# Performance work log

Measured on AMD Instinct MI355X. Metric: run time of the kernel, lower is better.

The kernel has to match this reference:

```python
import jax, jax.numpy as jnp
import numpy as np

N, FIN, HID, HEADS, DHEAD = 4096, 512, 256, 4, 256
TOPK = 29  # hard-coded t=29 in HAN1.forward
FOUT = HEADS * DHEAD  # 1024


def setup_inputs() -> dict:
    key = jax.random.key(0)
    ks = jax.random.split(key, 12)
    h = jax.random.normal(ks[0], (N, FIN), dtype=jnp.float32)
    simlar = jax.random.normal(ks[1], (N, N), dtype=jnp.float32)
    # binary adjacency, avg degree ~41 so top-k (29) actually prunes
    adj = (jax.random.uniform(ks[2], (N, N)) < 0.01).astype(jnp.float32)
    s = 0.05
    W_trans = jax.random.normal(ks[3], (FIN, HID), dtype=jnp.float32) * s
    gat_W = jax.random.normal(ks[4], (HID, FOUT), dtype=jnp.float32) * s
    attn_l = jax.random.normal(ks[5], (HEADS, DHEAD), dtype=jnp.float32) * s
    attn_r = jax.random.normal(ks[6], (HEADS, DHEAD), dtype=jnp.float32) * s
    gat_bias = jnp.zeros((FOUT,), dtype=jnp.float32)
    sem_W1 = jax.random.normal(ks[7], (FOUT, 128), dtype=jnp.float32) * s
    sem_b1 = jnp.zeros((128,), dtype=jnp.float32)
    sem_W2 = jax.random.normal(ks[8], (128, 1), dtype=jnp.float32) * s
    return {"h": h, "simlar": simlar, "adj": adj, "W_trans": W_trans,
            "gat_W": gat_W, "attn_l": attn_l, "attn_r": attn_r,
            "gat_bias": gat_bias, "sem_W1": sem_W1, "sem_b1": sem_b1,
            "sem_W2": sem_W2}


def reference(h, simlar, adj, W_trans, gat_W, attn_l, attn_r, gat_bias,
              sem_W1, sem_b1, sem_W2):
    lrelu01 = lambda x: jax.nn.leaky_relu(x, 0.01)  # nn.LeakyReLU default
    # ---- adjacency sparsification: per-row top-k of filtered similarity ----
    filt = lrelu01(adj * simlar) * (adj > 0).astype(adj.dtype)  # [N,N]
    top_vals, top_idx = jax.lax.top_k(filt, TOPK)               # [N,TOPK]
    rows = jnp.arange(N)[:, None]
    newmat = jnp.zeros_like(filt).at[rows, top_idx].set(top_vals)
    mask = newmat != 0  # mask[src, dst]: edge src->dst (nonzero() semantics)
    # ---- feature transform (dropout p=0 -> identity) ----
    x = lrelu01(h @ W_trans)                                    # [N,HID]
    # ---- GATConv (DGL semantics, negative_slope=0.2, activation=elu) ----
    feat = (x @ gat_W).reshape(N, HEADS, DHEAD)                 # [N,H,D]
    el = jnp.einsum('nhd,hd->nh', feat, attn_l)                 # src scores
    er = jnp.einsum('nhd,hd->nh', feat, attn_r)                 # dst scores
    e = jax.nn.leaky_relu(el[:, None, :] + er[None, :, :], 0.2) # [src,dst,H]
    mask3 = mask[:, :, None]
    e = jnp.where(mask3, e, jnp.asarray(-1e30, e.dtype))
    emax = jnp.max(e, axis=0, keepdims=True)
    exp_e = jnp.where(mask3, jnp.exp(e - emax), 0.0)
    denom = jnp.sum(exp_e, axis=0, keepdims=True)
    alpha = exp_e / jnp.maximum(denom, 1e-20)  # zero-in-degree -> zero output
    rst = jnp.einsum('sdh,shf->dhf', alpha, feat)               # [N,H,D]
    rst = jax.nn.elu(rst + gat_bias.reshape(HEADS, DHEAD))
    sem = rst.reshape(N, FOUT)                                  # flatten(1)
    # ---- semantic attention over meta-paths (here: 1 meta-path) ----
    z = sem[:, None, :]                                         # [N,1,F]
    w = (jnp.tanh(z @ sem_W1 + sem_b1) @ sem_W2).mean(0)        # [1,1]
    beta = jax.nn.softmax(w, axis=0)                            # [1,1]
    out = (beta[None, :, :] * z).sum(1)                         # [N,F]
    return out
```

## Files before the change

### kernel.cpp

```cpp
#include <hip/hip_runtime.h>
#include <hip/hip_bf16.h>
#include <math.h>

#define N 4096
#define FIN 512
#define HID 256
#define HEADS 4
#define DHEAD 256
#define FOUT 1024
#define TOPK 29
#define CAP 64
#define CAPC 96

typedef __attribute__((ext_vector_type(8))) short short8;
typedef __attribute__((ext_vector_type(4))) float f32x4;
typedef __hip_bfloat16 bf16;

__device__ __forceinline__ float bflo(unsigned int u) {
  return __uint_as_float(u << 16);
}
__device__ __forceinline__ float bfhi(unsigned int u) {
  return __uint_as_float(u & 0xffff0000u);
}

__global__ __launch_bounds__(256) void prep_kernel(
    const float* __restrict__ h, const float* __restrict__ W_trans,
    const float* __restrict__ gat_W, const float* __restrict__ attn_l,
    const float* __restrict__ attn_r, bf16* __restrict__ hb,
    bf16* __restrict__ Wtb, bf16* __restrict__ gWtb,
    float* __restrict__ alr2, int* __restrict__ colcnt) {
  const int S1 = 4096;
  const int S2 = S1 + N * FIN / 4;
  const int S3 = S2 + HID * FIN / 4;
  const int S4 = S3 + FOUT * HID / 4;
  const int TOT = S4 + 2 * HEADS * HID * 16;
  const int stride = gridDim.x * 256;
  for (int i = blockIdx.x * 256 + threadIdx.x; i < TOT; i += stride) {
    if (i < S1) {
      colcnt[i] = 0;
    } else if (i < S2) {
      const int j = i - S1;
      const float4 v = reinterpret_cast<const float4*>(h)[j];
      bf16 tmp[4];
      tmp[0] = __float2bfloat16(v.x);
      tmp[1] = __float2bfloat16(v.y);
      tmp[2] = __float2bfloat16(v.z);
      tmp[3] = __float2bfloat16(v.w);
      *reinterpret_cast<ushort4*>(&hb[(size_t)j * 4]) =
          *reinterpret_cast<ushort4*>(tmp);
    } else if (i < S3) {
      const int j4 = i - S2;
      const float4 v = reinterpret_cast<const float4*>(W_trans)[j4];
      const int k = j4 >> 6;
      const int c0 = (j4 & 63) * 4;
      Wtb[(size_t)(c0 + 0) * FIN + k] = __float2bfloat16(v.x);
      Wtb[(size_t)(c0 + 1) * FIN + k] = __float2bfloat16(v.y);
      Wtb[(size_t)(c0 + 2) * FIN + k] = __float2bfloat16(v.z);
      Wtb[(size_t)(c0 + 3) * FIN + k] = __float2bfloat16(v.w);
    } else if (i < S4) {
      const int j4 = i - S3;
      const float4 v = reinterpret_cast<const float4*>(gat_W)[j4];
      const int k = j4 >> 8;
      const int c0 = (j4 & 255) * 4;
      gWtb[(size_t)(c0 + 0) * HID + k] = __float2bfloat16(v.x);
      gWtb[(size_t)(c0 + 1) * HID + k] = __float2bfloat16(v.y);
      gWtb[(size_t)(c0 + 2) * HID + k] = __float2bfloat16(v.z);
      gWtb[(size_t)(c0 + 3) * HID + k] = __float2bfloat16(v.w);
    } else {
      const int u = i - S4;
      const int j = u >> 4, l16 = u & 15;
      const float* vec = (j < 1024) ? attn_l : attn_r;
      const int jj = j & 1023;
      const int hh = jj >> 8, k = jj & 255;
      const float4* wp = reinterpret_cast<const float4*>(
          &gat_W[(size_t)k * FOUT + hh * DHEAD + l16 * 16]);
      const float4* vp = reinterpret_cast<const float4*>(&vec[hh * DHEAD + l16 * 16]);
      float acc = 0.f;
#pragma unroll
      for (int q = 0; q < 4; ++q) {
        const float4 w4 = wp[q], v4 = vp[q];
        acc += w4.x * v4.x + w4.y * v4.y + w4.z * v4.z + w4.w * v4.w;
      }
#pragma unroll
      for (int off = 1; off < 16; off <<= 1) acc += __shfl_xor(acc, off);
      if (l16 == 0) alr2[j] = acc;
    }
  }
}

__global__ __launch_bounds__(256) void rowscan_kernel(const float* __restrict__ adj,
                                                      const float* __restrict__ simlar,
                                                      int* __restrict__ colcnt,
                                                      int* __restrict__ colsrc) {
  const int t = threadIdx.x, s = blockIdx.x;
  __shared__ float swv[CAP];
  __shared__ int swi[CAP];
  __shared__ int cnt;
  if (t == 0) cnt = 0;
  __syncthreads();
  const uint4* rowadj = reinterpret_cast<const uint4*>(adj + (size_t)s * N);
  const float4* rowsim = reinterpret_cast<const float4*>(simlar + (size_t)s * N);
  uint4 a[4];
#pragma unroll
  for (int q = 0; q < 4; ++q) a[q] = rowadj[q * 256 + t];
  unsigned any = 0;
#pragma unroll
  for (int q = 0; q < 4; ++q) any |= a[q].x | a[q].y | a[q].z | a[q].w;
  if (any) {
#pragma unroll
    for (int q = 0; q < 4; ++q) {
      if (a[q].x | a[q].y | a[q].z | a[q].w) {
        const int j = q * 256 + t;
        const float4 s4 = rowsim[j];
        const unsigned aw[4] = {a[q].x, a[q].y, a[q].z, a[q].w};
        const float ss[4] = {s4.x, s4.y, s4.z, s4.w};
#pragma unroll
        for (int c = 0; c < 4; ++c) {
          if (aw[c] && ss[c] > 0.f) {
            const int p = atomicAdd(&cnt, 1);
            if (p < CAP) {
              swv[p] = ss[c];
              swi[p] = j * 4 + c;
            }
          }
        }
      }
    }
  }
  __syncthreads();
  const int C = min(cnt, CAP);
  if (t < C) {
    const float x = swv[t];
    int rk = 0;
    for (int jj = 0; jj < C; ++jj) rk += (swv[jj] > x);
    if (rk < TOPK) {
      const int d = swi[t];
      const int p = atomicAdd(&colcnt[d], 1);
      if (p < CAPC) colsrc[(size_t)d * CAPC + p] = s;
    }
  }
}

__global__ __launch_bounds__(256) void gemm_mfma64(const bf16* __restrict__ A,
                                                   const bf16* __restrict__ Bt,
                                                   bf16* __restrict__ Cb,
                                                   int M, int Nn, int K) {
  __shared__ bf16 As[64][72];
  __shared__ bf16 Bs[64][72];
  const int t = threadIdx.x;
  const int bm = blockIdx.x * 64, bn = blockIdx.y * 64;
  const int w = t >> 6, lane = t & 63, r = lane & 15, g = lane >> 4;
  const int m = t >> 2, c0 = (t & 3) * 8;
  f32x4 acc[4] = {};
  for (int k0 = 0; k0 < K; k0 += 64) {
    const bf16* arow = &A[(size_t)(bm + m) * K + k0];
    const bf16* brow = &Bt[(size_t)(bn + m) * K + k0];
    *reinterpret_cast<int4*>(&As[m][c0]) = *reinterpret_cast<const int4*>(&arow[c0]);
    *reinterpret_cast<int4*>(&As[m][c0 + 32]) = *reinterpret_cast<const int4*>(&arow[c0 + 32]);
    *reinterpret_cast<int4*>(&Bs[m][c0]) = *reinterpret_cast<const int4*>(&brow[c0]);
    *reinterpret_cast<int4*>(&Bs[m][c0 + 32]) = *reinterpret_cast<const int4*>(&brow[c0 + 32]);
    __syncthreads();
    const short8 a0 = *reinterpret_cast<short8*>(&As[w * 16 + r][g * 8]);
    const short8 a1 = *reinterpret_cast<short8*>(&As[w * 16 + r][32 + g * 8]);
#pragma unroll
    for (int j = 0; j < 4; ++j) {
      const short8 b0 = *reinterpret_cast<short8*>(&Bs[j * 16 + r][g * 8]);
      const short8 b1 = *reinterpret_cast<short8*>(&Bs[j * 16 + r][32 + g * 8]);
      acc[j] = __builtin_amdgcn_mfma_f32_16x16x32_bf16(a0, b0, acc[j], 0, 0, 0);
      acc[j] = __builtin_amdgcn_mfma_f32_16x16x32_bf16(a1, b1, acc[j], 0, 0, 0);
    }
    __syncthreads();
  }
#pragma unroll
  for (int j = 0; j < 4; ++j)
#pragma unroll
    for (int q = 0; q < 4; ++q) {
      const int row = bm + w * 16 + g * 4 + q;
      const int col = bn + j * 16 + r;
      float v = acc[j][q];
      v = v >= 0.f ? v : 0.01f * v;
      Cb[(size_t)row * Nn + col] = __float2bfloat16(v);
    }
}

__global__ __launch_bounds__(256) void gemm_mfma128(const bf16* __restrict__ A,
                                                    const bf16* __restrict__ Bt,
                                                    bf16* __restrict__ Cb,
                                                    int M, int Nn, int K) {
  __shared__ bf16 As[128][40];
  __shared__ bf16 Bs[128][40];
  const int t = threadIdx.x;
  const int bm = blockIdx.x * 128, bn = blockIdx.y * 128;
  const int w = t >> 6, lane = t & 63, r = lane & 15, g = lane >> 4;
  const int m = t >> 1, c0 = (t & 1) * 16;
  f32x4 acc[2][8] = {};
  for (int k0 = 0; k0 < K; k0 += 32) {
    const bf16* arow = &A[(size_t)(bm + m) * K + k0 + c0];
    const bf16* brow = &Bt[(size_t)(bn + m) * K + k0 + c0];
    *reinterpret_cast<int4*>(&As[m][c0]) = *reinterpret_cast<const int4*>(arow);
    *reinterpret_cast<int4*>(&As[m][c0 + 8]) = *reinterpret_cast<const int4*>(arow + 8);
    *reinterpret_cast<int4*>(&Bs[m][c0]) = *reinterpret_cast<const int4*>(brow);
    *reinterpret_cast<int4*>(&Bs[m][c0 + 8]) = *reinterpret_cast<const int4*>(brow + 8);
    __syncthreads();
    const short8 a0 = *reinterpret_cast<short8*>(&As[w * 32 + r][g * 8]);
    const short8 a1 = *reinterpret_cast<short8*>(&As[w * 32 + 16 + r][g * 8]);
#pragma unroll
    for (int j = 0; j < 8; ++j) {
      const short8 b = *reinterpret_cast<short8*>(&Bs[j * 16 + r][g * 8]);
      acc[0][j] = __builtin_amdgcn_mfma_f32_16x16x32_bf16(a0, b, acc[0][j], 0, 0, 0);
      acc[1][j] = __builtin_amdgcn_mfma_f32_16x16x32_bf16(a1, b, acc[1][j], 0, 0, 0);
    }
    __syncthreads();
  }
#pragma unroll
  for (int i = 0; i < 2; ++i)
#pragma unroll
    for (int j = 0; j < 8; ++j)
#pragma unroll
      for (int q = 0; q < 4; ++q) {
        const int row = bm + w * 32 + i * 16 + g * 4 + q;
        const int col = bn + j * 16 + r;
        Cb[(size_t)row * Nn + col] = __float2bfloat16(acc[i][j][q]);
      }
}

__global__ __launch_bounds__(256) void elr2_kernel(const bf16* __restrict__ xb,
                                                   const float* __restrict__ alr2,
                                                   float* __restrict__ el,
                                                   float* __restrict__ er) {
  __shared__ float alrs[2048];
  const int t = threadIdx.x;
  for (int i = t; i < 2048; i += 256) alrs[i] = alr2[i];
  __syncthreads();
  const int wv = t >> 6, lane = t & 63;
  const int n = blockIdx.x * 4 + wv;
  const uint2 v2 = *reinterpret_cast<const uint2*>(&xb[(size_t)n * HID + lane * 4]);
  const float xf[4] = {bflo(v2.x), bfhi(v2.x), bflo(v2.y), bfhi(v2.y)};
  float pl[4], pr[4];
#pragma unroll
  for (int hh = 0; hh < 4; ++hh) {
    const int base = hh * 256 + lane * 4;
    pl[hh] = xf[0] * alrs[base] + xf[1] * alrs[base + 1] +
             xf[2] * alrs[base + 2] + xf[3] * alrs[base + 3];
    pr[hh] = xf[0] * alrs[1024 + base] + xf[1] * alrs[1024 + base + 1] +
             xf[2] * alrs[1024 + base + 2] + xf[3] * alrs[1024 + base + 3];
  }
  for (int off = 32; off; off >>= 1) {
#pragma unroll
    for (int hh = 0; hh < 4; ++hh) {
      pl[hh] += __shfl_xor(pl[hh], off);
      pr[hh] += __shfl_xor(pr[hh], off);
    }
  }
  if (lane == 0) {
#pragma unroll
    for (int hh = 0; hh < 4; ++hh) {
      el[n * HEADS + hh] = pl[hh];
      er[n * HEADS + hh] = pr[hh];
    }
  }
}

__global__ __launch_bounds__(256) void agg_kernel(const int* __restrict__ colcnt,
                                                  const int* __restrict__ colsrc,
                                                  const float* __restrict__ el,
                                                  const float* __restrict__ er,
                                                  const bf16* __restrict__ featb,
                                                  const float* __restrict__ bias,
                                                  float* __restrict__ out) {
  __shared__ int tmp[4][CAPC];
  __shared__ int slist[4][CAPC];
  __shared__ float pbuf[4][2][CAPC];
  const int t = threadIdx.x;
  const int grp = t >> 6;
  const int lane = t & 63;
  const int hf = blockIdx.x & 1;
  const int d = (blockIdx.x >> 1) * 4 + grp;
  const int C = min(colcnt[d], CAPC);
  for (int i = lane; i < C; i += 64) tmp[grp][i] = colsrc[(size_t)d * CAPC + i];
  __syncthreads();
  for (int i = lane; i < C; i += 64) {
    const int v = tmp[grp][i];
    int rk = 0;
    for (int j = 0; j < C; ++j) rk += (tmp[grp][j] < v);
    slist[grp][rk] = v;
  }
  __syncthreads();
  const int sl = lane >> 5;
  const int h = hf * 2 + sl;
  const int hl = lane & 31;
  const float er_dh = er[d * HEADS + h];
  float m = -INFINITY;
  for (int i = hl; i < C; i += 32) {
    float e = el[slist[grp][i] * HEADS + h] + er_dh;
    e = e >= 0.f ? e : 0.2f * e;
    pbuf[grp][sl][i] = e;
    m = fmaxf(m, e);
  }
#pragma unroll
  for (int off = 16; off; off >>= 1) m = fmaxf(m, __shfl_xor(m, off));
  float dsum = 0.f;
  for (int i = hl; i < C; i += 32) {
    const float p = __expf(pbuf[grp][sl][i] - m);
    pbuf[grp][sl][i] = p;
    dsum += p;
  }
#pragma unroll
  for (int off = 16; off; off >>= 1) dsum += __shfl_xor(dsum, off);
  __syncthreads();
  const size_t dimoff = hf * 512 + lane * 8;
  float acc[8] = {};
  int i = 0;
  for (; i + 2 <= C; i += 2) {
    const float p0 = pbuf[grp][sl][i];
    const float p1 = pbuf[grp][sl][i + 1];
    const uint4 v0 = *reinterpret_cast<const uint4*>(
        &featb[(size_t)slist[grp][i] * FOUT + dimoff]);
    const uint4 v1 = *reinterpret_cast<const uint4*>(
        &featb[(size_t)slist[grp][i + 1] * FOUT + dimoff]);
    acc[0] = fmaf(p0, bflo(v0.x), acc[0]);
    acc[1] = fmaf(p0, bfhi(v0.x), acc[1]);
    acc[2] = fmaf(p0, bflo(v0.y), acc[2]);
    acc[3] = fmaf(p0, bfhi(v0.y), acc[3]);
    acc[4] = fmaf(p0, bflo(v0.z), acc[4]);
    acc[5] = fmaf(p0, bfhi(v0.z), acc[5]);
    acc[6] = fmaf(p0, bflo(v0.w), acc[6]);
    acc[7] = fmaf(p0, bfhi(v0.w), acc[7]);
    acc[0] = fmaf(p1, bflo(v1.x), acc[0]);
    acc[1] = fmaf(p1, bfhi(v1.x), acc[1]);
    acc[2] = fmaf(p1, bflo(v1.y), acc[2]);
    acc[3] = fmaf(p1, bfhi(v1.y), acc[3]);
    acc[4] = fmaf(p1, bflo(v1.z), acc[4]);
    acc[5] = fmaf(p1, bfhi(v1.z), acc[5]);
    acc[6] = fmaf(p1, bflo(v1.w), acc[6]);
    acc[7] = fmaf(p1, bfhi(v1.w), acc[7]);
  }
  if (i < C) {
    const float p0 = pbuf[grp][sl][i];
    const uint4 v0 = *reinterpret_cast<const uint4*>(
        &featb[(size_t)slist[grp][i] * FOUT + dimoff]);
    acc[0] = fmaf(p0, bflo(v0.x), acc[0]);
    acc[1] = fmaf(p0, bfhi(v0.x), acc[1]);
    acc[2] = fmaf(p0, bflo(v0.y), acc[2]);
    acc[3] = fmaf(p0, bfhi(v0.y), acc[3]);
    acc[4] = fmaf(p0, bflo(v0.z), acc[4]);
    acc[5] = fmaf(p0, bfhi(v0.z), acc[5]);
    acc[6] = fmaf(p0, bflo(v0.w), acc[6]);
    acc[7] = fmaf(p0, bfhi(v0.w), acc[7]);
  }
  const float inv = C > 0 ? 1.f / dsum : 0.f;
  float o[8];
#pragma unroll
  for (int k = 0; k < 8; ++k) {
    const float r = acc[k] * inv + bias[dimoff + k];
    o[k] = r > 0.f ? r : expm1f(r);
  }
  float* op = &out[(size_t)d * FOUT + dimoff];
  *reinterpret_cast<float4*>(op) = make_float4(o[0], o[1], o[2], o[3]);
  *reinterpret_cast<float4*>(op + 4) = make_float4(o[4], o[5], o[6], o[7]);
}

extern "C" void kernel_launch(void* const* d_in, const int* in_sizes, int n_in,
                              void* d_out, int out_size, void* d_ws, size_t ws_size,
                              hipStream_t stream) {
  const float* h        = (const float*)d_in[0];
  const float* simlar   = (const float*)d_in[1];
  const float* adj      = (const float*)d_in[2];
  const float* W_trans  = (const float*)d_in[3];
  const float* gat_W    = (const float*)d_in[4];
  const float* attn_l   = (const float*)d_in[5];
  const float* attn_r   = (const float*)d_in[6];
  const float* gat_bias = (const float*)d_in[7];
  float* out = (float*)d_out;

  char* ws = (char*)d_ws;
  const size_t MB = 1 << 20;
  bf16* hb    = (bf16*)(ws);
  bf16* Wtb   = (bf16*)(ws + 4 * MB);
  bf16* gWtb  = (bf16*)(ws + 4 * MB + 512 * 1024);
  bf16* xb    = (bf16*)(ws + 5 * MB);
  float* el   = (float*)(ws + 7 * MB);
  float* er   = (float*)(ws + 7 * MB + 65536);
  float* alr2 = (float*)(ws + 7 * MB + 131072);
  bf16* featb = (bf16*)(ws + 8 * MB);
  int* colcnt = (int*)(ws + 16 * MB);
  int* colsrc = (int*)(ws + 17 * MB);

  prep_kernel<<<2048, 256, 0, stream>>>(h, W_trans, gat_W, attn_l, attn_r,
                                        hb, Wtb, gWtb, alr2, colcnt);
  rowscan_kernel<<<N, 256, 0, stream>>>(adj, simlar, colcnt, colsrc);
  gemm_mfma64<<<dim3(N / 64, HID / 64), 256, 0, stream>>>(hb, Wtb, xb, N, HID, FIN);
  gemm_mfma128<<<dim3(N / 128, FOUT / 128), 256, 0, stream>>>(xb, gWtb, featb, N, FOUT, HID);
  elr2_kernel<<<N / 4, 256, 0, stream>>>(xb, alr2, el, er);
  agg_kernel<<<N / 2, 256, 0, stream>>>(colcnt, colsrc, el, er, featb, gat_bias, out);
}
```

Before: 75.46 us.

## Fuse prep into rowscan, convert h in GEMM, head-major feat layout

Merges the weight-transpose and attention-vector prep work into the row-scan kernel, which removes one launch. It also drops the separate fp32-to-bf16 pass over h by converting on the fly in the first GEMM's load. The second GEMM now uses a K-tile of 64 and writes feat head-major, so each aggregation block handles one head with 64 lanes reading 4 contiguous bf16 values. Several __syncthreads are removed from agg because each wave owns its own slot. The trade-off is that the first GEMM reloads fp32 h for every column tile, and agg launches twice as many blocks, each doing narrower gathers.

```diff
diff --git a/kernel.cpp b/kernel.cpp
--- a/kernel.cpp
+++ b/kernel.cpp
@@ -23,76 +23,62 @@
   return __uint_as_float(u & 0xffff0000u);
 }
 
-__global__ __launch_bounds__(256) void prep_kernel(
-    const float* __restrict__ h, const float* __restrict__ W_trans,
-    const float* __restrict__ gat_W, const float* __restrict__ attn_l,
-    const float* __restrict__ attn_r, bf16* __restrict__ hb,
+__global__ __launch_bounds__(256) void scan_kernel(
+    const float* __restrict__ W_trans, const float* __restrict__ gat_W,
+    const float* __restrict__ attn_l, const float* __restrict__ attn_r,
+    const float* __restrict__ adj, const float* __restrict__ simlar,
     bf16* __restrict__ Wtb, bf16* __restrict__ gWtb,
-    float* __restrict__ alr2, int* __restrict__ colcnt) {
-  const int S1 = 4096;
-  const int S2 = S1 + N * FIN / 4;
-  const int S3 = S2 + HID * FIN / 4;
-  const int S4 = S3 + FOUT * HID / 4;
-  const int TOT = S4 + 2 * HEADS * HID * 16;
-  const int stride = gridDim.x * 256;
-  for (int i = blockIdx.x * 256 + threadIdx.x; i < TOT; i += stride) {
-    if (i < S1) {
-      colcnt[i] = 0;
-    } else if (i < S2) {
-      const int j = i - S1;
-      const float4 v = reinterpret_cast<const float4*>(h)[j];
-      bf16 tmp[4];
-      tmp[0] = __float2bfloat16(v.x);
-      tmp[1] = __float2bfloat16(v.y);
-      tmp[2] = __float2bfloat16(v.z);
-      tmp[3] = __float2bfloat16(v.w);
-      *reinterpret_cast<ushort4*>(&hb[(size_t)j * 4]) =
-          *reinterpret_cast<ushort4*>(tmp);
-    } else if (i < S3) {
-      const int j4 = i - S2;
-      const float4 v = reinterpret_cast<const float4*>(W_trans)[j4];
-      const int k = j4 >> 6;
-      const int c0 = (j4 & 63) * 4;
-      Wtb[(size_t)(c0 + 0) * FIN + k] = __float2bfloat16(v.x);
-      Wtb[(size_t)(c0 + 1) * FIN + k] = __float2bfloat16(v.y);
-      Wtb[(size_t)(c0 + 2) * FIN + k] = __float2bfloat16(v.z);
-      Wtb[(size_t)(c0 + 3) * FIN + k] = __float2bfloat16(v.w);
-    } else if (i < S4) {
-      const int j4 = i - S3;
-      const float4 v = reinterpret_cast<const float4*>(gat_W)[j4];
-      const int k = j4 >> 8;
-      const int c0 = (j4 & 255) * 4;
-      gWtb[(size_t)(c0 + 0) * HID + k] = __float2bfloat16(v.x);
-      gWtb[(size_t)(c0 + 1) * HID + k] = __float2bfloat16(v.y);
-      gWtb[(size_t)(c0 + 2) * HID + k] = __float2bfloat16(v.z);
-      gWtb[(size_t)(c0 + 3) * HID + k] = __float2bfloat16(v.w);
-    } else {
-      const int u = i - S4;
-      const int j = u >> 4, l16 = u & 15;
-      const float* vec = (j < 1024) ? attn_l : attn_r;
-      const int jj = j & 1023;
-      const int hh = jj >> 8, k = jj & 255;
-      const float4* wp = reinterpret_cast<const float4*>(
-          &gat_W[(size_t)k * FOUT + hh * DHEAD + l16 * 16]);
-      const float4* vp = reinterpret_cast<const float4*>(&vec[hh * DHEAD + l16 * 16]);
-      float acc = 0.f;
-#pragma unroll
-      for (int q = 0; q < 4; ++q) {
-        const float4 w4 = wp[q], v4 = vp[q];
-        acc += w4.x * v4.x + w4.y * v4.y + w4.z * v4.z + w4.w * v4.w;
+    float* __restrict__ alr2, int* __restrict__ colcnt,
+    int* __restrict__ colsrc) {
+  const int t = threadIdx.x, s = blockIdx.x;
+  {
+    const int S1 = 4096;
+    const int S2 = S1 + HID * FIN / 4;
+    const int S3 = S2 + FOUT * HID / 4;
+    const int TOT = S3 + 2 * HEADS * HID * 16;
+    const int i = s * 256 + t;
+    if (i < TOT) {
+      if (i < S1) {
+        colcnt[i] = 0;
+      } else if (i < S2) {
+        const int j4 = i - S1;
+        const float4 v = reinterpret_cast<const float4*>(W_trans)[j4];
+        const int k = j4 >> 6;
+        const int c0 = (j4 & 63) * 4;
+        Wtb[(size_t)(c0 + 0) * FIN + k] = __float2bfloat16(v.x);
+        Wtb[(size_t)(c0 + 1) * FIN + k] = __float2bfloat16(v.y);
+        Wtb[(size_t)(c0 + 2) * FIN + k] = __float2bfloat16(v.z);
+        Wtb[(size_t)(c0 + 3) * FIN + k] = __float2bfloat16(v.w);
+      } else if (i < S3) {
+        const int j4 = i - S2;
+        const float4 v = reinterpret_cast<const float4*>(gat_W)[j4];
+        const int k = j4 >> 8;
+        const int c0 = (j4 & 255) * 4;
+        gWtb[(size_t)(c0 + 0) * HID + k] = __float2bfloat16(v.x);
+        gWtb[(size_t)(c0 + 1) * HID + k] = __float2bfloat16(v.y);
+        gWtb[(size_t)(c0 + 2) * HID + k] = __float2bfloat16(v.z);
+        gWtb[(size_t)(c0 + 3) * HID + k] = __float2bfloat16(v.w);
+      } else {
+        const int u = i - S3;
+        const int j = u >> 4, l16 = u & 15;
+        const float* vec = (j < 1024) ? attn_l : attn_r;
+        const int jj = j & 1023;
+        const int hh = jj >> 8, k = jj & 255;
+        const float4* wp = reinterpret_cast<const float4*>(
+            &gat_W[(size_t)k * FOUT + hh * DHEAD + l16 * 16]);
+        const float4* vp = reinterpret_cast<const float4*>(&vec[hh * DHEAD + l16 * 16]);
+        float acc = 0.f;
+#pragma unroll
+        for (int q = 0; q < 4; ++q) {
+          const float4 w4 = wp[q], v4 = vp[q];
+          acc += w4.x * v4.x + w4.y * v4.y + w4.z * v4.z + w4.w * v4.w;
+        }
+#pragma unroll
+        for (int off = 1; off < 16; off <<= 1) acc += __shfl_xor(acc, off);
+        if (l16 == 0) alr2[j] = acc;
       }
-#pragma unroll
-      for (int off = 1; off < 16; off <<= 1) acc += __shfl_xor(acc, off);
-      if (l16 == 0) alr2[j] = acc;
-    }
-  }
-}
-
-__global__ __launch_bounds__(256) void rowscan_kernel(const float* __restrict__ adj,
-                                                      const float* __restrict__ simlar,
-                                                      int* __restrict__ colcnt,
-                                                      int* __restrict__ colsrc) {
-  const int t = threadIdx.x, s = blockIdx.x;
+    }
+  }
   __shared__ float swv[CAP];
   __shared__ int swi[CAP];
   __shared__ int cnt;
@@ -141,24 +127,39 @@
   }
 }
 
-__global__ __launch_bounds__(256) void gemm_mfma64(const bf16* __restrict__ A,
-                                                   const bf16* __restrict__ Bt,
-                                                   bf16* __restrict__ Cb,
-                                                   int M, int Nn, int K) {
+__global__ __launch_bounds__(256) void gemm_h(const float* __restrict__ A,
+                                              const bf16* __restrict__ Bt,
+                                              bf16* __restrict__ Cb) {
   __shared__ bf16 As[64][72];
   __shared__ bf16 Bs[64][72];
   const int t = threadIdx.x;
   const int bm = blockIdx.x * 64, bn = blockIdx.y * 64;
   const int w = t >> 6, lane = t & 63, r = lane & 15, g = lane >> 4;
-  const int m = t >> 2, c0 = (t & 3) * 8;
+  const int m = t >> 2;
+  const int fb = (t & 3) * 16;
+  const int c0 = (t & 3) * 8;
   f32x4 acc[4] = {};
-  for (int k0 = 0; k0 < K; k0 += 64) {
-    const bf16* arow = &A[(size_t)(bm + m) * K + k0];
-    const bf16* brow = &Bt[(size_t)(bn + m) * K + k0];
-    *reinterpret_cast<int4*>(&As[m][c0]) = *reinterpret_cast<const int4*>(&arow[c0]);
-    *reinterpret_cast<int4*>(&As[m][c0 + 32]) = *reinterpret_cast<const int4*>(&arow[c0 + 32]);
-    *reinterpret_cast<int4*>(&Bs[m][c0]) = *reinterpret_cast<const int4*>(&brow[c0]);
-    *reinterpret_cast<int4*>(&Bs[m][c0 + 32]) = *reinterpret_cast<const int4*>(&brow[c0 + 32]);
+  for (int k0 = 0; k0 < FIN; k0 += 64) {
+    {
+      const float4* hp = reinterpret_cast<const float4*>(&A[(size_t)(bm + m) * FIN + k0 + fb]);
+      const float4 f0 = hp[0], f1 = hp[1], f2 = hp[2], f3 = hp[3];
+      bf16 ta[16];
+      ta[0] = __float2bfloat16(f0.x); ta[1] = __float2bfloat16(f0.y);
+      ta[2] = __float2bfloat16(f0.z); ta[3] = __float2bfloat16(f0.w);
+      ta[4] = __float2bfloat16(f1.x); ta[5] = __float2bfloat16(f1.y);
+      ta[6] = __float2bfloat16(f1.z); ta[7] = __float2bfloat16(f1.w);
+      ta[8] = __float2bfloat16(f2.x); ta[9] = __float2bfloat16(f2.y);
+      ta[10] = __float2bfloat16(f2.z); ta[11] = __float2bfloat16(f2.w);
+      ta[12] = __float2bfloat16(f3.x); ta[13] = __float2bfloat16(f3.y);
+      ta[14] = __float2bfloat16(f3.z); ta[15] = __float2bfloat16(f3.w);
+      *reinterpret_cast<int4*>(&As[m][fb]) = *reinterpret_cast<int4*>(&ta[0]);
+      *reinterpret_cast<int4*>(&As[m][fb + 8]) = *reinterpret_cast<int4*>(&ta[8]);
+    }
+    {
+      const bf16* brow = &Bt[(size_t)(bn + m) * FIN + k0];
+      *reinterpret_cast<int4*>(&Bs[m][c0]) = *reinterpret_cast<const int4*>(&brow[c0]);
+      *reinterpret_cast<int4*>(&Bs[m][c0 + 32]) = *reinterpret_cast<const int4*>(&brow[c0 + 32]);
+    }
     __syncthreads();
     const short8 a0 = *reinterpret_cast<short8*>(&As[w * 16 + r][g * 8]);
     const short8 a1 = *reinterpret_cast<short8*>(&As[w * 16 + r][32 + g * 8]);
@@ -179,39 +180,48 @@
       const int col = bn + j * 16 + r;
       float v = acc[j][q];
       v = v >= 0.f ? v : 0.01f * v;
-      Cb[(size_t)row * Nn + col] = __float2bfloat16(v);
-    }
-}
-
-__global__ __launch_bounds__(256) void gemm_mfma128(const bf16* __restrict__ A,
-                                                    const bf16* __restrict__ Bt,
-                                                    bf16* __restrict__ Cb,
-                                                    int M, int Nn, int K) {
-  __shared__ bf16 As[128][40];
-  __shared__ bf16 Bs[128][40];
+      Cb[(size_t)row * HID + col] = __float2bfloat16(v);
+    }
+}
+
+__global__ __launch_bounds__(256) void gemm128(const bf16* __restrict__ A,
+                                               const bf16* __restrict__ Bt,
+                                               bf16* __restrict__ Cb) {
+  __shared__ bf16 As[128][72];
+  __shared__ bf16 Bs[128][72];
   const int t = threadIdx.x;
   const int bm = blockIdx.x * 128, bn = blockIdx.y * 128;
   const int w = t >> 6, lane = t & 63, r = lane & 15, g = lane >> 4;
-  const int m = t >> 1, c0 = (t & 1) * 16;
+  const int m = t >> 1, cb = (t & 1) * 32;
   f32x4 acc[2][8] = {};
-  for (int k0 = 0; k0 < K; k0 += 32) {
-    const bf16* arow = &A[(size_t)(bm + m) * K + k0 + c0];
-    const bf16* brow = &Bt[(size_t)(bn + m) * K + k0 + c0];
-    *reinterpret_cast<int4*>(&As[m][c0]) = *reinterpret_cast<const int4*>(arow);
-    *reinterpret_cast<int4*>(&As[m][c0 + 8]) = *reinterpret_cast<const int4*>(arow + 8);
-    *reinterpret_cast<int4*>(&Bs[m][c0]) = *reinterpret_cast<const int4*>(brow);
-    *reinterpret_cast<int4*>(&Bs[m][c0 + 8]) = *reinterpret_cast<const int4*>(brow + 8);
+  for (int k0 = 0; k0 < HID; k0 += 64) {
+    const bf16* arow = &A[(size_t)(bm + m) * HID + k0 + cb];
+    const bf16* brow = &Bt[(size_t)(bn + m) * HID + k0 + cb];
+#pragma unroll
+    for (int q = 0; q < 4; ++q) {
+      *reinterpret_cast<int4*>(&As[m][cb + q * 8]) =
+          *reinterpret_cast<const int4*>(&arow[q * 8]);
+      *reinterpret_cast<int4*>(&Bs[m][cb + q * 8]) =
+          *reinterpret_cast<const int4*>(&brow[q * 8]);
+    }
     __syncthreads();
-    const short8 a0 = *reinterpret_cast<short8*>(&As[w * 32 + r][g * 8]);
-    const short8 a1 = *reinterpret_cast<short8*>(&As[w * 32 + 16 + r][g * 8]);
+    const short8 a00 = *reinterpret_cast<short8*>(&As[w * 32 + r][g * 8]);
+    const short8 a01 = *reinterpret_cast<short8*>(&As[w * 32 + r][32 + g * 8]);
+    const short8 a10 = *reinterpret_cast<short8*>(&As[w * 32 + 16 + r][g * 8]);
+    const short8 a11 = *reinterpret_cast<short8*>(&As[w * 32 + 16 + r][32 + g * 8]);
 #pragma unroll
     for (int j = 0; j < 8; ++j) {
-      const short8 b = *reinterpret_cast<short8*>(&Bs[j * 16 + r][g * 8]);
-      acc[0][j] = __builtin_amdgcn_mfma_f32_16x16x32_bf16(a0, b, acc[0][j], 0, 0, 0);
-      acc[1][j] = __builtin_amdgcn_mfma_f32_16x16x32_bf16(a1, b, acc[1][j], 0, 0, 0);
+      const short8 b0 = *reinterpret_cast<short8*>(&Bs[j * 16 + r][g * 8]);
+      const short8 b1 = *reinterpret_cast<short8*>(&Bs[j * 16 + r][32 + g * 8]);
+      acc[0][j] = __builtin_amdgcn_mfma_f32_16x16x32_bf16(a00, b0, acc[0][j], 0, 0, 0);
+      acc[0][j] = __builtin_amdgcn_mfma_f32_16x16x32_bf16(a01, b1, acc[0][j], 0, 0, 0);
+      acc[1][j] = __builtin_amdgcn_mfma_f32_16x16x32_bf16(a10, b0, acc[1][j], 0, 0, 0);
+      acc[1][j] = __builtin_amdgcn_mfma_f32_16x16x32_bf16(a11, b1, acc[1][j], 0, 0, 0);
     }
     __syncthreads();
   }
+  const int hh = bn >> 8;
+  const int dbase = bn & 255;
 #pragma unroll
   for (int i = 0; i < 2; ++i)
 #pragma unroll
@@ -219,8 +229,8 @@
 #pragma unroll
       for (int q = 0; q < 4; ++q) {
         const int row = bm + w * 32 + i * 16 + g * 4 + q;
-        const int col = bn + j * 16 + r;
-        Cb[(size_t)row * Nn + col] = __float2bfloat16(acc[i][j][q]);
+        const int dd = dbase + j * 16 + r;
+        Cb[((size_t)hh * N + row) * DHEAD + dd] = __float2bfloat16(acc[i][j][q]);
       }
 }
 
@@ -270,94 +280,77 @@
                                                   float* __restrict__ out) {
   __shared__ int tmp[4][CAPC];
   __shared__ int slist[4][CAPC];
-  __shared__ float pbuf[4][2][CAPC];
+  __shared__ float pbuf[4][CAPC];
   const int t = threadIdx.x;
   const int grp = t >> 6;
   const int lane = t & 63;
-  const int hf = blockIdx.x & 1;
-  const int d = (blockIdx.x >> 1) * 4 + grp;
+  const int h = blockIdx.x & 3;
+  const int d = (blockIdx.x >> 2) * 4 + grp;
   const int C = min(colcnt[d], CAPC);
   for (int i = lane; i < C; i += 64) tmp[grp][i] = colsrc[(size_t)d * CAPC + i];
-  __syncthreads();
   for (int i = lane; i < C; i += 64) {
     const int v = tmp[grp][i];
     int rk = 0;
     for (int j = 0; j < C; ++j) rk += (tmp[grp][j] < v);
     slist[grp][rk] = v;
   }
-  __syncthreads();
-  const int sl = lane >> 5;
-  const int h = hf * 2 + sl;
-  const int hl = lane & 31;
   const float er_dh = er[d * HEADS + h];
   float m = -INFINITY;
-  for (int i = hl; i < C; i += 32) {
+  for (int i = lane; i < C; i += 64) {
     float e = el[slist[grp][i] * HEADS + h] + er_dh;
     e = e >= 0.f ? e : 0.2f * e;
-    pbuf[grp][sl][i] = e;
+    pbuf[grp][i] = e;
     m = fmaxf(m, e);
   }
 #pragma unroll
-  for (int off = 16; off; off >>= 1) m = fmaxf(m, __shfl_xor(m, off));
+  for (int off = 32; off; off >>= 1) m = fmaxf(m, __shfl_xor(m, off));
   float dsum = 0.f;
-  for (int i = hl; i < C; i += 32) {
-    const float p = __expf(pbuf[grp][sl][i] - m);
-    pbuf[grp][sl][i] = p;
+  for (int i = lane; i < C; i += 64) {
+    const float p = __expf(pbuf[grp][i] - m);
+    pbuf[grp][i] = p;
     dsum += p;
   }
 #pragma unroll
-  for (int off = 16; off; off >>= 1) dsum += __shfl_xor(dsum, off);
-  __syncthreads();
-  const size_t dimoff = hf * 512 + lane * 8;
-  float acc[8] = {};
+  for (int off = 32; off; off >>= 1) dsum += __shfl_xor(dsum, off);
+  const bf16* fh = featb + (size_t)h * N * DHEAD;
+  float a0 = 0.f, a1 = 0.f, a2 = 0.f, a3 = 0.f;
   int i = 0;
   for (; i + 2 <= C; i += 2) {
-    const float p0 = pbuf[grp][sl][i];
-    const float p1 = pbuf[grp][sl][i + 1];
-    const uint4 v0 = *reinterpret_cast<const uint4*>(
-        &featb[(size_t)slist[grp][i] * FOUT + dimoff]);
-    const uint4 v1 = *reinterpret_cast<const uint4*>(
-        &featb[(size_t)slist[grp][i + 1] * FOUT + dimoff]);
-    acc[0] = fmaf(p0, bflo(v0.x), acc[0]);
-    acc[1] = fmaf(p0, bfhi(v0.x), acc[1]);
-    acc[2] = fmaf(p0, bflo(v0.y), acc[2]);
-    acc[3] = fmaf(p0, bfhi(v0.y), acc[3]);
-    acc[4] = fmaf(p0, bflo(v0.z), acc[4]);
-    acc[5] = fmaf(p0, bfhi(v0.z), acc[5]);
-    acc[6] = fmaf(p0, bflo(v0.w), acc[6]);
-    acc[7] = fmaf(p0, bfhi(v0.w), acc[7]);
-    acc[0] = fmaf(p1, bflo(v1.x), acc[0]);
-    acc[1] = fmaf(p1, bfhi(v1.x), acc[1]);
-    acc[2] = fmaf(p1, bflo(v1.y), acc[2]);
-    acc[3] = fmaf(p1, bfhi(v1.y), acc[3]);
-    acc[4] = fmaf(p1, bflo(v1.z), acc[4]);
-    acc[5] = fmaf(p1, bfhi(v1.z), acc[5]);
-    acc[6] = fmaf(p1, bflo(v1.w), acc[6]);
-    acc[7] = fmaf(p1, bfhi(v1.w), acc[7]);
+    const float p0 = pbuf[grp][i];
+    const float p1 = pbuf[grp][i + 1];
+    const uint2 v0 = *reinterpret_cast<const uint2*>(
+        &fh[(size_t)slist[grp][i] * DHEAD + lane * 4]);
+    const uint2 v1 = *reinterpret_cast<const uint2*>(
+        &fh[(size_t)slist[grp][i + 1] * DHEAD + lane * 4]);
+    a0 = fmaf(p0, bflo(v0.x), a0);
+    a1 = fmaf(p0, bfhi(v0.x), a1);
+    a2 = fmaf(p0, bflo(v0.y), a2);
+    a3 = fmaf(p0, bfhi(v0.y), a3);
+    a0 = fmaf(p1, bflo(v1.x), a0);
+    a1 = fmaf(p1, bfhi(v1.x), a1);
+    a2 = fmaf(p1, bflo(v1.y), a2);
+    a3 = fmaf(p1, bfhi(v1.y), a3);
   }
   if (i < C) {
-    const float p0 = pbuf[grp][sl][i];
-    const uint4 v0 = *reinterpret_cast<const uint4*>(
-        &featb[(size_t)slist[grp][i] * FOUT + dimoff]);
-    acc[0] = fmaf(p0, bflo(v0.x), acc[0]);
-    acc[1] = fmaf(p0, bfhi(v0.x), acc[1]);
-    acc[2] = fmaf(p0, bflo(v0.y), acc[2]);
-    acc[3] = fmaf(p0, bfhi(v0.y), acc[3]);
-    acc[4] = fmaf(p0, bflo(v0.z), acc[4]);
-    acc[5] = fmaf(p0, bfhi(v0.z), acc[5]);
-    acc[6] = fmaf(p0, bflo(v0.w), acc[6]);
-    acc[7] = fmaf(p0, bfhi(v0.w), acc[7]);
+    const float p0 = pbuf[grp][i];
+    const uint2 v0 = *reinterpret_cast<const uint2*>(
+        &fh[(size_t)slist[grp][i] * DHEAD + lane * 4]);
+    a0 = fmaf(p0, bflo(v0.x), a0);
+    a1 = fmaf(p0, bfhi(v0.x), a1);
+    a2 = fmaf(p0, bflo(v0.y), a2);
+    a3 = fmaf(p0, bfhi(v0.y), a3);
   }
   const float inv = C > 0 ? 1.f / dsum : 0.f;
-  float o[8];
-#pragma unroll
-  for (int k = 0; k < 8; ++k) {
-    const float r = acc[k] * inv + bias[dimoff + k];
-    o[k] = r > 0.f ? r : expm1f(r);
-  }
-  float* op = &out[(size_t)d * FOUT + dimoff];
-  *reinterpret_cast<float4*>(op) = make_float4(o[0], o[1], o[2], o[3]);
-  *reinterpret_cast<float4*>(op + 4) = make_float4(o[4], o[5], o[6], o[7]);
+  const int dbase = h * DHEAD + lane * 4;
+  float o[4];
+  o[0] = a0 * inv + bias[dbase + 0];
+  o[1] = a1 * inv + bias[dbase + 1];
+  o[2] = a2 * inv + bias[dbase + 2];
+  o[3] = a3 * inv + bias[dbase + 3];
+#pragma unroll
+  for (int k = 0; k < 4; ++k) o[k] = o[k] > 0.f ? o[k] : expm1f(o[k]);
+  *reinterpret_cast<float4*>(&out[(size_t)d * FOUT + dbase]) =
+      make_float4(o[0], o[1], o[2], o[3]);
 }
 
 extern "C" void kernel_launch(void* const* d_in, const int* in_sizes, int n_in,
@@ -375,22 +368,20 @@
 
   char* ws = (char*)d_ws;
   const size_t MB = 1 << 20;
-  bf16* hb    = (bf16*)(ws);
-  bf16* Wtb   = (bf16*)(ws + 4 * MB);
-  bf16* gWtb  = (bf16*)(ws + 4 * MB + 512 * 1024);
-  bf16* xb    = (bf16*)(ws + 5 * MB);
-  float* el   = (float*)(ws + 7 * MB);
-  float* er   = (float*)(ws + 7 * MB + 65536);
-  float* alr2 = (float*)(ws + 7 * MB + 131072);
-  bf16* featb = (bf16*)(ws + 8 * MB);
-  int* colcnt = (int*)(ws + 16 * MB);
-  int* colsrc = (int*)(ws + 17 * MB);
-
-  prep_kernel<<<2048, 256, 0, stream>>>(h, W_trans, gat_W, attn_l, attn_r,
-                                        hb, Wtb, gWtb, alr2, colcnt);
-  rowscan_kernel<<<N, 256, 0, stream>>>(adj, simlar, colcnt, colsrc);
-  gemm_mfma64<<<dim3(N / 64, HID / 64), 256, 0, stream>>>(hb, Wtb, xb, N, HID, FIN);
-  gemm_mfma128<<<dim3(N / 128, FOUT / 128), 256, 0, stream>>>(xb, gWtb, featb, N, FOUT, HID);
+  bf16* Wtb   = (bf16*)(ws);
+  bf16* gWtb  = (bf16*)(ws + 512 * 1024);
+  bf16* xb    = (bf16*)(ws + 1 * MB);
+  float* el   = (float*)(ws + 3 * MB);
+  float* er   = (float*)(ws + 3 * MB + 65536);
+  float* alr2 = (float*)(ws + 3 * MB + 131072);
+  bf16* featb = (bf16*)(ws + 4 * MB);
+  int* colcnt = (int*)(ws + 12 * MB);
+  int* colsrc = (int*)(ws + 13 * MB);
+
+  scan_kernel<<<N, 256, 0, stream>>>(W_trans, gat_W, attn_l, attn_r, adj, simlar,
+                                     Wtb, gWtb, alr2, colcnt, colsrc);
+  gemm_h<<<dim3(N / 64, HID / 64), 256, 0, stream>>>(h, Wtb, xb);
+  gemm128<<<dim3(N / 128, FOUT / 128), 256, 0, stream>>>(xb, gWtb, featb);
   elr2_kernel<<<N / 4, 256, 0, stream>>>(xb, alr2, el, er);
-  agg_kernel<<<N / 2, 256, 0, stream>>>(colcnt, colsrc, el, er, featb, gat_bias, out);
-}
+  agg_kernel<<<N, 256, 0, stream>>>(colcnt, colsrc, el, er, featb, gat_bias, out);
+}
```

After: 67.11 us. 1.12x faster.
